# Kernel optimization log

Hardware: AMD Instinct MI355X
Metric: run time of the kernel (lower is better)

The kernel has to match this reference:

```python
import jax, jax.numpy as jnp
import numpy as np

B, Q, C, N, H, W = 2, 4096, 256, 6, 64, 96
HEADS, POINTS = 8, 4


def _grid_sample(img, grid):
    # img: [G, C, H, W]; grid: [G, P, 2] in [-1,1]
    # bilinear, align_corners=False, padding_mode='zeros' (matches F.grid_sample)
    G, Cc, Hh, Ww = img.shape
    gx = (grid[..., 0] + 1.0) * (Ww / 2.0) - 0.5
    gy = (grid[..., 1] + 1.0) * (Hh / 2.0) - 0.5
    x0f = jnp.floor(gx)
    y0f = jnp.floor(gy)
    wx = (gx - x0f)[:, None, :]
    wy = (gy - y0f)[:, None, :]
    x0 = x0f.astype(jnp.int32)
    y0 = y0f.astype(jnp.int32)
    flat = img.reshape(G, Cc, Hh * Ww)

    def gather(xi, yi):
        valid = ((xi >= 0) & (xi < Ww) & (yi >= 0) & (yi < Hh))
        idx = jnp.clip(yi, 0, Hh - 1) * Ww + jnp.clip(xi, 0, Ww - 1)
        v = jnp.take_along_axis(flat, idx[:, None, :], axis=2)  # [G,C,P]
        return v * valid[:, None, :].astype(img.dtype)

    v00 = gather(x0, y0)
    v01 = gather(x0 + 1, y0)
    v10 = gather(x0, y0 + 1)
    v11 = gather(x0 + 1, y0 + 1)
    return (v00 * (1 - wx) * (1 - wy) + v01 * wx * (1 - wy)
            + v10 * (1 - wx) * wy + v11 * wx * wy)


def setup_inputs() -> dict:
    key = jax.random.key(0)
    ks = jax.random.split(key, 12)
    query = jax.random.normal(ks[0], (B, Q, C), dtype=jnp.float32)
    query_coords = jax.random.uniform(ks[1], (B, Q, 3), dtype=jnp.float32)
    image_feats = jax.random.normal(ks[2], (B, N, C, H, W), dtype=jnp.float32)
    # realistic f-theta fisheye intrinsics for 1280x1080 images
    Kmat = np.array([[500.0, 0.0, 640.0], [0.0, 500.0, 540.0], [0.0, 0.0, 1.0]], dtype=np.float32)
    intrinsics = jnp.asarray(np.tile(Kmat, (B, N, 1, 1)))
    # inverse extrinsics: identity rotation, cameras 3m behind the voxel volume (cam_z > 0)
    E = np.tile(np.eye(4, dtype=np.float32), (B, N, 1, 1))
    for n in range(N):
        E[:, n, 0, 3] = 0.2 * n - 0.5
        E[:, n, 2, 3] = 3.0
    inv_extrinsics = jnp.asarray(E)
    s = 1.0 / np.sqrt(C)
    W_off = jax.random.normal(ks[3], (C, N * HEADS * POINTS * 2), dtype=jnp.float32) * 0.02
    b_off = jnp.zeros((N * HEADS * POINTS * 2,), dtype=jnp.float32)
    W_attn = jax.random.normal(ks[4], (C, N * HEADS * POINTS), dtype=jnp.float32) * s
    b_attn = jnp.zeros((N * HEADS * POINTS,), dtype=jnp.float32)
    W_val = jax.random.normal(ks[5], (C, C), dtype=jnp.float32) * s
    b_val = jax.random.normal(ks[6], (C,), dtype=jnp.float32) * 0.01
    W_out = jax.random.normal(ks[7], (C, C), dtype=jnp.float32) * s
    b_out = jax.random.normal(ks[8], (C,), dtype=jnp.float32) * 0.01
    return {"query": query, "query_coords": query_coords, "image_feats": image_feats,
            "intrinsics": intrinsics, "inv_extrinsics": inv_extrinsics,
            "W_off": W_off, "b_off": b_off, "W_attn": W_attn, "b_attn": b_attn,
            "W_val": W_val, "b_val": b_val, "W_out": W_out, "b_out": b_out}


def reference(query, query_coords, image_feats, intrinsics, inv_extrinsics,
              W_off, b_off, W_attn, b_attn, W_val, b_val, W_out, b_out):
    Bq, Qq, Cq = query.shape
    _, Nn, _, Hh, Ww = image_feats.shape
    hd = Cq // HEADS
    # ---- reference points: voxel coords -> world -> camera -> f-theta image ----
    xmin, ymin, zmin, xmax, ymax, zmax = -3.6, -3.0, -0.7, 3.6, 3.0, 2.5
    rx = query_coords[..., 0] * (xmax - xmin) + xmin
    ry = query_coords[..., 1] * (ymax - ymin) + ymin
    rz = query_coords[..., 2] * (zmax - zmin) + zmin
    world = jnp.stack([rx, ry, rz, jnp.ones_like(rx)], axis=-1)  # [B,Q,4]
    cam = jnp.einsum('bnij,bqj->bnqi', inv_extrinsics, world)    # [B,N,Q,4]
    cxp, cyp, czp = cam[..., 0], cam[..., 1], cam[..., 2]
    r3d = jnp.sqrt(cxp * cxp + cyp * cyp + 1e-8)
    theta = jnp.arctan2(r3d, czp)
    phi = jnp.arctan2(cyp, cxp)
    fx = intrinsics[:, :, 0, 0][..., None]
    cx0 = intrinsics[:, :, 0, 2][..., None]
    cy0 = intrinsics[:, :, 1, 2][..., None]
    r_img = fx * theta
    u = r_img * jnp.cos(phi) + cx0
    v = r_img * jnp.sin(phi) + cy0
    origH, origW = 1080, 1280
    ref = jnp.stack([2.0 * u / (origW - 1) - 1.0, 2.0 * v / (origH - 1) - 1.0], axis=-1)  # [B,N,Q,2]
    fov = ((czp > 0) & (theta < 1.372)).astype(query.dtype)      # [B,N,Q]
    # ---- offsets + attention weights ----
    offs = jnp.tanh((query @ W_off + b_off).reshape(Bq, Qq, Nn, HEADS, POINTS, 2)) * 0.5
    aw = (query @ W_attn + b_attn).reshape(Bq, Qq, Nn, HEADS, POINTS)
    aw = aw * jnp.transpose(fov, (0, 2, 1))[..., None, None]
    aw = jax.nn.softmax(aw, axis=-1)
    # ---- value projection ----
    val = jnp.einsum('bnchw,cd->bnhwd', image_feats, W_val) + b_val  # [B,N,H,W,C]
    val = val.reshape(Bq, Nn, Hh, Ww, HEADS, hd)
    # ---- sampling locations ----
    locs = ref[:, :, :, None, None, :] + jnp.transpose(offs, (0, 2, 1, 3, 4, 5))  # [B,N,Q,h,p,2]
    v_all = jnp.transpose(val, (0, 1, 4, 5, 2, 3)).reshape(Bq * Nn * HEADS, hd, Hh, Ww)
    locs_all = jnp.transpose(locs, (0, 1, 3, 2, 4, 5)).reshape(Bq * Nn * HEADS, Qq * POINTS, 2)
    sampled = _grid_sample(v_all, locs_all).reshape(Bq, Nn, HEADS, hd, Qq, POINTS)
    sampled = jnp.transpose(sampled, (0, 4, 1, 2, 5, 3))  # [B,Q,N,heads,points,hd]
    weighted = jnp.sum(sampled * aw[..., None], axis=4)   # [B,Q,N,heads,hd]
    out = weighted.sum(axis=2).reshape(Bq, Qq, Cq)
    return out @ W_out + b_out
```

## Files before the change

kernel.cpp:

```cpp
#include <hip/hip_runtime.h>
#include <math.h>

#define Bb 2
#define Qq 4096
#define Cc 256
#define Nn 6
#define Hh 64
#define Ww 96
#define HEADS 8
#define POINTS 4
#define HW (Hh*Ww)
#define BQ (Bb*Qq)

#define WS_VAL   0
#define WS_WTF   9437184
#define WS_WCHF  9469952
#define WS_WCLF  9543680
#define WS_WOTF  9617408
#define WS_LOCS  18874368
#define WS_AW    22020096
#define WS_REFF  23592960
#define WS_WSUM  23740416

typedef __attribute__((ext_vector_type(8))) short short8;
typedef __attribute__((ext_vector_type(4))) float f32x4;

__device__ __forceinline__ unsigned short f2bf(float f) {
    union { float f; unsigned u; } v; v.f = f;
    unsigned r = (v.u + 0x7fffu + ((v.u >> 16) & 1u)) >> 16;
    return (unsigned short)r;
}
__device__ __forceinline__ float bf2f(unsigned short h) { return __uint_as_float((unsigned)h << 16); }
__device__ __forceinline__ float bflo(unsigned u) { return __uint_as_float(u << 16); }
__device__ __forceinline__ float bfhi(unsigned u) { return __uint_as_float(u & 0xffff0000u); }
__device__ __forceinline__ unsigned packbf(float a, float b) {
    return (unsigned)f2bf(a) | ((unsigned)f2bf(b) << 16);
}

__global__ void prep_kernel(const float* __restrict__ qc,
                            const float* __restrict__ intr,
                            const float* __restrict__ invE,
                            float* __restrict__ reff,
                            const float* __restrict__ Wv,
                            const float* __restrict__ Wo,
                            const float* __restrict__ Wa,
                            const float* __restrict__ Wu,
                            unsigned short* __restrict__ Wtf,
                            unsigned short* __restrict__ Wchf,
                            unsigned short* __restrict__ Wclf,
                            unsigned short* __restrict__ Wotf) {
    int blk = blockIdx.x;
    int tid = threadIdx.x;
    if (blk < 32) {
        int idx = blk * 256 + tid;
        int b = idx >> 12;
        int q = idx & (Qq - 1);
        float rx = qc[idx*3+0] * 7.2f - 3.6f;
        float ry = qc[idx*3+1] * 6.0f - 3.0f;
        float rz = qc[idx*3+2] * 3.2f - 0.7f;
        for (int n = 0; n < Nn; ++n) {
            const float* E = invE + (b*Nn+n)*16;
            float camx = E[0]*rx + E[1]*ry + E[2]*rz  + E[3];
            float camy = E[4]*rx + E[5]*ry + E[6]*rz  + E[7];
            float camz = E[8]*rx + E[9]*ry + E[10]*rz + E[11];
            const float* K = intr + (b*Nn+n)*9;
            float fx = K[0], cx0 = K[2], cy0 = K[5];
            float r3d   = sqrtf(camx*camx + camy*camy + 1e-8f);
            float theta = atan2f(r3d, camz);
            float phi   = atan2f(camy, camx);
            float r_img = fx * theta;
            float u = r_img * cosf(phi) + cx0;
            float v = r_img * sinf(phi) + cy0;
            int base = ((b*Nn+n)*Qq + q)*3;
            reff[base+0] = 2.0f * u / 1279.0f - 1.0f;
            reff[base+1] = 2.0f * v / 1079.0f - 1.0f;
            reff[base+2] = (camz > 0.0f && theta < 1.372f) ? 1.0f : 0.0f;
        }
        return;
    }
    int idx = (blk - 32) * 256 + tid;
    if (idx < 65536) {
        int s = idx & 7, l = (idx >> 3) & 63, kk = (idx >> 9) & 7, t = idx >> 12;
        int n = t*16 + (l & 15);
        int k = kk*32 + (l >> 4)*8 + s;
        Wtf[idx] = f2bf(Wv[k*256 + n]);
    } else if (idx < 212992) {
        int i2 = idx - 65536;
        int s = i2 & 7, l = (i2 >> 3) & 63, kk = (i2 >> 9) & 7, t = i2 >> 12;
        int n = t*16 + (l & 15);
        int k = kk*32 + (l >> 4)*8 + s;
        float w = (n < 384) ? Wo[k*384 + n] : Wa[k*192 + (n - 384)];
        unsigned short h = f2bf(w);
        Wchf[i2] = h;
        Wclf[i2] = f2bf(w - bf2f(h));
    } else {
        int i3 = idx - 212992;
        int s = i3 & 7, l = (i3 >> 3) & 63, kk = (i3 >> 9) & 7, t = i3 >> 12;
        int n = t*16 + (l & 15);
        int k = kk*32 + (l >> 4)*8 + s;
        Wotf[i3] = f2bf(Wu[k*256 + n]);
    }
}

__global__ __launch_bounds__(512, 2) void vp_mfma_kernel(const float* __restrict__ feats,
                                                         const unsigned short* __restrict__ Wtf,
                                                         const float* __restrict__ bv,
                                                         unsigned short* __restrict__ val) {
    __shared__ __align__(16) unsigned short As[64 * 272];
    int t = threadIdx.x;
    int pix0 = blockIdx.x * 64;
    int bn = blockIdx.y;
    const float* A = feats + (size_t)bn * Cc * HW + pix0;
    int lane = t & 63, wavei = t >> 6, quad = lane >> 4, l15 = lane & 15;
    {
        int pq = t & 15;
        int oct = t >> 4;
        float va[8][4];
#pragma unroll
        for (int j = 0; j < 8; ++j)
            *(float4*)va[j] = *(const float4*)&A[(size_t)(oct*8 + j)*HW + pq*4];
#pragma unroll
        for (int e = 0; e < 4; ++e) {
            int m = pq*4 + e;
            uint4 pk;
            pk.x = packbf(va[0][e], va[1][e]);
            pk.y = packbf(va[2][e], va[3][e]);
            pk.z = packbf(va[4][e], va[5][e]);
            pk.w = packbf(va[6][e], va[7][e]);
            *(uint4*)&As[m*264 + oct*8] = pk;
        }
    }
    __syncthreads();
    int wm = wavei & 1;
    int wn = wavei >> 1;
    int r0 = wm*32 + l15, r1 = r0 + 16;
    const unsigned short* Wl = Wtf + (size_t)lane * 8;
#define VP_BOFF(nt, kk) ((size_t)(((wn*4 + (nt))*8 + (kk)) << 9))
    f32x4 acc[2][4];
#pragma unroll
    for (int i = 0; i < 2; ++i)
#pragma unroll
        for (int j = 0; j < 4; ++j) acc[i][j] = (f32x4){0.f, 0.f, 0.f, 0.f};
    short8 bA[4], bB[4];
#pragma unroll
    for (int nt = 0; nt < 4; ++nt) bA[nt] = *(const short8*)&Wl[VP_BOFF(nt, 0)];
#pragma unroll
    for (int kk = 0; kk < 8; kk += 2) {
        if (kk + 1 < 8) {
#pragma unroll
            for (int nt = 0; nt < 4; ++nt) bB[nt] = *(const short8*)&Wl[VP_BOFF(nt, kk+1)];
        }
        {
            short8 a0 = *(const short8*)&As[r0*264 + kk*32 + quad*8];
            short8 a1 = *(const short8*)&As[r1*264 + kk*32 + quad*8];
#pragma unroll
            for (int nt = 0; nt < 4; ++nt) {
                acc[0][nt] = __builtin_amdgcn_mfma_f32_16x16x32_bf16(a0, bA[nt], acc[0][nt], 0, 0, 0);
                acc[1][nt] = __builtin_amdgcn_mfma_f32_16x16x32_bf16(a1, bA[nt], acc[1][nt], 0, 0, 0);
            }
        }
        if (kk + 2 < 8) {
#pragma unroll
            for (int nt = 0; nt < 4; ++nt) bA[nt] = *(const short8*)&Wl[VP_BOFF(nt, kk+2)];
        }
        if (kk + 1 < 8) {
            int k1 = kk + 1;
            short8 a0 = *(const short8*)&As[r0*264 + k1*32 + quad*8];
            short8 a1 = *(const short8*)&As[r1*264 + k1*32 + quad*8];
#pragma unroll
            for (int nt = 0; nt < 4; ++nt) {
                acc[0][nt] = __builtin_amdgcn_mfma_f32_16x16x32_bf16(a0, bB[nt], acc[0][nt], 0, 0, 0);
                acc[1][nt] = __builtin_amdgcn_mfma_f32_16x16x32_bf16(a1, bB[nt], acc[1][nt], 0, 0, 0);
            }
        }
    }
    __syncthreads();
#pragma unroll
    for (int nt = 0; nt < 4; ++nt) {
        int n = wn*64 + nt*16 + l15;
        float bias = bv[n];
#pragma unroll
        for (int mt = 0; mt < 2; ++mt) {
#pragma unroll
            for (int r = 0; r < 4; ++r) {
                int mm = wm*32 + mt*16 + quad*4 + r;
                As[mm*272 + n] = f2bf(acc[mt][nt][r] + bias);
            }
        }
    }
    __syncthreads();
#pragma unroll
    for (int i = 0; i < 4; ++i) {
        int flat = wavei*2048 + i*512 + lane*8;
        int pix = flat >> 8, ch = flat & 255;
        int head = ch >> 5, c32 = ch & 31;
        *(uint4*)&val[(((size_t)bn*HEADS + head)*HW + pix0 + pix)*32 + c32] =
            *(const uint4*)&As[pix*272 + ch];
    }
}

__global__ __launch_bounds__(512, 4) void qp_kernel(const float* __restrict__ query,
                                                    const unsigned short* __restrict__ Wchf,
                                                    const unsigned short* __restrict__ Wclf,
                                                    const float* __restrict__ b_off,
                                                    const float* __restrict__ b_attn,
                                                    const float* __restrict__ reff,
                                                    float* __restrict__ locs,
                                                    float* __restrict__ aw) {
    __shared__ __align__(16) unsigned short Ah[32 * 256];
    __shared__ __align__(16) unsigned short Al[32 * 256];
    int t = threadIdx.x;
    int row0 = blockIdx.x * 32;
    int ty = blockIdx.y;
    {
        int row = t & 31;
        int c2 = t >> 5;
        const float* src = query + (size_t)(row0 + row) * 256;
#pragma unroll
        for (int cc = 0; cc < 2; ++cc) {
            int c = c2 * 2 + cc;
            float4 v0 = *(const float4*)&src[c*8 + 0];
            float4 v1 = *(const float4*)&src[c*8 + 4];
            float f[8] = {v0.x, v0.y, v0.z, v0.w, v1.x, v1.y, v1.z, v1.w};
            unsigned short h[8], l[8];
#pragma unroll
            for (int j = 0; j < 8; ++j) {
                h[j] = f2bf(f[j]);
                l[j] = f2bf(f[j] - bf2f(h[j]));
            }
            uint4 ph, pl;
            ph.x = h[0] | ((unsigned)h[1] << 16); ph.y = h[2] | ((unsigned)h[3] << 16);
            ph.z = h[4] | ((unsigned)h[5] << 16); ph.w = h[6] | ((unsigned)h[7] << 16);
            pl.x = l[0] | ((unsigned)l[1] << 16); pl.y = l[2] | ((unsigned)l[3] << 16);
            pl.z = l[4] | ((unsigned)l[5] << 16); pl.w = l[6] | ((unsigned)l[7] << 16);
            int pos = row * 256 + ((c ^ row) << 3);
            *(uint4*)&Ah[pos] = ph;
            *(uint4*)&Al[pos] = pl;
        }
    }
    __syncthreads();
    int wave = t >> 6, lane = t & 63, quad = lane >> 4, l15 = lane & 15;
    int ms = wave & 1;
    int ng = wave >> 1;
    int arow = ms*16 + l15;
    int bq = row0 >> 12;
    int tile0 = ty*12 + ng*3;
    f32x4 acc[3];
#pragma unroll
    for (int i = 0; i < 3; ++i) acc[i] = (f32x4){0.f, 0.f, 0.f, 0.f};

#define QP_FB(i, kk) (((size_t)((tile0 + (i))*8 + (kk)) << 9) + lane*8)

    if (ty < 2) {
        short8 bhA[3], blA[3], bhB[3], blB[3];
#pragma unroll
        for (int i = 0; i < 3; ++i) {
            bhA[i] = *(const short8*)&Wchf[QP_FB(i, 0)];
            blA[i] = *(const short8*)&Wclf[QP_FB(i, 0)];
        }
#pragma unroll
        for (int kk = 0; kk < 8; kk += 2) {
            if (kk + 1 < 8) {
#pragma unroll
                for (int i = 0; i < 3; ++i) {
                    bhB[i] = *(const short8*)&Wchf[QP_FB(i, kk+1)];
                    blB[i] = *(const short8*)&Wclf[QP_FB(i, kk+1)];
                }
            }
            {
                int apos = arow*256 + (((kk*4+quad) ^ arow) << 3);
                short8 a_h = *(const short8*)&Ah[apos];
                short8 a_l = *(const short8*)&Al[apos];
#pragma unroll
                for (int i = 0; i < 3; ++i) {
                    acc[i] = __builtin_amdgcn_mfma_f32_16x16x32_bf16(a_h, bhA[i], acc[i], 0, 0, 0);
                    acc[i] = __builtin_amdgcn_mfma_f32_16x16x32_bf16(a_l, bhA[i], acc[i], 0, 0, 0);
                    acc[i] = __builtin_amdgcn_mfma_f32_16x16x32_bf16(a_h, blA[i], acc[i], 0, 0, 0);
                }
            }
            if (kk + 2 < 8) {
#pragma unroll
                for (int i = 0; i < 3; ++i) {
                    bhA[i] = *(const short8*)&Wchf[QP_FB(i, kk+2)];
                    blA[i] = *(const short8*)&Wclf[QP_FB(i, kk+2)];
                }
            }
            if (kk + 1 < 8) {
                int k1 = kk + 1;
                int apos = arow*256 + (((k1*4+quad) ^ arow) << 3);
                short8 a_h = *(const short8*)&Ah[apos];
                short8 a_l = *(const short8*)&Al[apos];
#pragma unroll
                for (int i = 0; i < 3; ++i) {
                    acc[i] = __builtin_amdgcn_mfma_f32_16x16x32_bf16(a_h, bhB[i], acc[i], 0, 0, 0);
                    acc[i] = __builtin_amdgcn_mfma_f32_16x16x32_bf16(a_l, bhB[i], acc[i], 0, 0, 0);
                    acc[i] = __builtin_amdgcn_mfma_f32_16x16x32_bf16(a_h, blB[i], acc[i], 0, 0, 0);
                }
            }
        }
#pragma unroll
        for (int i = 0; i < 3; ++i) {
            int j = (tile0 + i)*16 + l15;
            int n_cam = j >> 6;
            int xy = j & 1;
            float bias = b_off[j];
#pragma unroll
            for (int r = 0; r < 4; ++r) {
                int q = row0 + ms*16 + quad*4 + r;
                int qq = q & (Qq-1);
                float refv = reff[((bq*Nn + n_cam)*Qq + qq)*3 + xy];
                locs[(size_t)q*384 + j] = refv + tanhf(acc[i][r] + bias) * 0.5f;
            }
        }
    } else {
        short8 bhA[3], bhB[3];
#pragma unroll
        for (int i = 0; i < 3; ++i) bhA[i] = *(const short8*)&Wchf[QP_FB(i, 0)];
#pragma unroll
        for (int kk = 0; kk < 8; kk += 2) {
            if (kk + 1 < 8) {
#pragma unroll
                for (int i = 0; i < 3; ++i) bhB[i] = *(const short8*)&Wchf[QP_FB(i, kk+1)];
            }
            {
                int apos = arow*256 + (((kk*4+quad) ^ arow) << 3);
                short8 a_h = *(const short8*)&Ah[apos];
#pragma unroll
                for (int i = 0; i < 3; ++i)
                    acc[i] = __builtin_amdgcn_mfma_f32_16x16x32_bf16(a_h, bhA[i], acc[i], 0, 0, 0);
            }
            if (kk + 2 < 8) {
#pragma unroll
                for (int i = 0; i < 3; ++i) bhA[i] = *(const short8*)&Wchf[QP_FB(i, kk+2)];
            }
            if (kk + 1 < 8) {
                int k1 = kk + 1;
                int apos = arow*256 + (((k1*4+quad) ^ arow) << 3);
                short8 a_h = *(const short8*)&Ah[apos];
#pragma unroll
                for (int i = 0; i < 3; ++i)
                    acc[i] = __builtin_amdgcn_mfma_f32_16x16x32_bf16(a_h, bhB[i], acc[i], 0, 0, 0);
            }
        }
#pragma unroll
        for (int i = 0; i < 3; ++i) {
            int j2 = (tile0 + i)*16 + l15 - 384;
            int n_cam = j2 >> 5;
            float bias = b_attn[j2];
#pragma unroll
            for (int r = 0; r < 4; ++r) {
                int q = row0 + ms*16 + quad*4 + r;
                int qq = q & (Qq-1);
                float fov = reff[((bq*Nn + n_cam)*Qq + qq)*3 + 2];
                float lg = (acc[i][r] + bias) * fov;
                float mx = fmaxf(lg, __shfl_xor(lg, 1));
                mx = fmaxf(mx, __shfl_xor(mx, 2));
                float e = expf(lg - mx);
                float s = e + __shfl_xor(e, 1);
                s = s + __shfl_xor(s, 2);
                aw[(size_t)q*192 + j2] = e / s;
            }
        }
    }
#undef QP_FB
}

__global__ __launch_bounds__(256, 4) void samp_kernel(const unsigned short* __restrict__ val,
                                                      const float* __restrict__ locs,
                                                      const float* __restrict__ aw,
                                                      unsigned short* __restrict__ wsum) {
    __shared__ float swgt[4][4][200];
    __shared__ int   soff[4][4][200];
    int t = threadIdx.x, wv = t >> 6, lane = t & 63;
    int q = blockIdx.x * 4 + wv;
    int b = q >> 12;
#pragma unroll
    for (int j = 0; j < 3; ++j) {
        int s = lane + 64*j;
        float2 xy = *(const float2*)&locs[(size_t)q*384 + 2*s];
        float w = aw[(size_t)q*192 + s];
        float gx = (xy.x + 1.0f)*48.0f - 0.5f;
        float gy = (xy.y + 1.0f)*32.0f - 0.5f;
        float x0f = floorf(gx), y0f = floorf(gy);
        float wx = gx - x0f, wy = gy - y0f;
        int ix = (int)x0f, iy = (int)y0f;
        bool vx0 = (unsigned)ix       < (unsigned)Ww;
        bool vx1 = (unsigned)(ix + 1) < (unsigned)Ww;
        bool vy0 = (unsigned)iy       < (unsigned)Hh;
        bool vy1 = (unsigned)(iy + 1) < (unsigned)Hh;
        int ix0 = min(max(ix, 0), Ww-1), ix1 = min(max(ix+1, 0), Ww-1);
        int iy0 = min(max(iy, 0), Hh-1), iy1 = min(max(iy+1, 0), Hh-1);
        swgt[wv][0][s] = (vx0 && vy0) ? w*(1.0f-wx)*(1.0f-wy) : 0.0f;
        swgt[wv][1][s] = (vx1 && vy0) ? w*wx*(1.0f-wy)        : 0.0f;
        swgt[wv][2][s] = (vx0 && vy1) ? w*(1.0f-wx)*wy        : 0.0f;
        swgt[wv][3][s] = (vx1 && vy1) ? w*wx*wy               : 0.0f;
        soff[wv][0][s] = (iy0*Ww + ix0) * 64;
        soff[wv][1][s] = (iy0*Ww + ix1) * 64;
        soff[wv][2][s] = (iy1*Ww + ix0) * 64;
        soff[wv][3][s] = (iy1*Ww + ix1) * 64;
    }
    __syncthreads();
    int cg   = lane >> 5;
    int head = (lane >> 2) & 7;
    int oc   = lane & 3;
    const char* vbase = (const char*)val + (size_t)(b*Nn*HEADS + head)*HW*64 + oc*16;
    float a[8] = {0.f,0.f,0.f,0.f,0.f,0.f,0.f,0.f};
#pragma unroll
    for (int n = 0; n < Nn; ++n) {
        const char* vb = vbase + (size_t)n*HEADS*HW*64;
#pragma unroll
        for (int p = 0; p < POINTS; ++p) {
            int s = (n*HEADS + head)*POINTS + p;
            float w0 = swgt[wv][cg*2+0][s];
            float w1 = swgt[wv][cg*2+1][s];
            int   o0 = soff[wv][cg*2+0][s];
            int   o1 = soff[wv][cg*2+1][s];
            uint4 u0 = *(const uint4*)(vb + o0);
            uint4 u1 = *(const uint4*)(vb + o1);
            a[0] += w0*bflo(u0.x); a[1] += w0*bfhi(u0.x);
            a[2] += w0*bflo(u0.y); a[3] += w0*bfhi(u0.y);
            a[4] += w0*bflo(u0.z); a[5] += w0*bfhi(u0.z);
            a[6] += w0*bflo(u0.w); a[7] += w0*bfhi(u0.w);
            a[0] += w1*bflo(u1.x); a[1] += w1*bfhi(u1.x);
            a[2] += w1*bflo(u1.y); a[3] += w1*bfhi(u1.y);
            a[4] += w1*bflo(u1.z); a[5] += w1*bfhi(u1.z);
            a[6] += w1*bflo(u1.w); a[7] += w1*bfhi(u1.w);
        }
    }
#pragma unroll
    for (int j = 0; j < 8; ++j) a[j] += __shfl_xor(a[j], 32);
    if (cg == 0) {
        int c = head*32 + oc*8;
        uint4 o;
        o.x = packbf(a[0], a[1]);
        o.y = packbf(a[2], a[3]);
        o.z = packbf(a[4], a[5]);
        o.w = packbf(a[6], a[7]);
        *(uint4*)&wsum[(size_t)q*256 + c] = o;
    }
}

__global__ __launch_bounds__(256) void out_mfma_kernel(const unsigned short* __restrict__ wsum,
                                                       const unsigned short* __restrict__ Wotf,
                                                       const float* __restrict__ b_out,
                                                       float* __restrict__ out) {
    int t = threadIdx.x;
    int row0 = blockIdx.x * 64;
    int col0 = blockIdx.y * 128;
    int wave = t >> 6, lane = t & 63, quad = lane >> 4, l15 = lane & 15;
    int wm = wave & 1;
    int wn = wave >> 1;
    f32x4 acc[2][4];
#pragma unroll
    for (int i = 0; i < 2; ++i)
#pragma unroll
        for (int j = 0; j < 4; ++j) acc[i][j] = (f32x4){0.f, 0.f, 0.f, 0.f};
#pragma unroll
    for (int kk = 0; kk < 8; ++kk) {
        short8 a[2];
#pragma unroll
        for (int mt = 0; mt < 2; ++mt)
            a[mt] = *(const short8*)&wsum[(size_t)(row0 + wm*32 + mt*16 + l15)*256 + kk*32 + quad*8];
#pragma unroll
        for (int nt = 0; nt < 4; ++nt) {
            size_t fb = ((size_t)((blockIdx.y*8 + wn*4 + nt)*8 + kk) << 9) + lane*8;
            short8 bfr = *(const short8*)&Wotf[fb];
            acc[0][nt] = __builtin_amdgcn_mfma_f32_16x16x32_bf16(a[0], bfr, acc[0][nt], 0, 0, 0);
            acc[1][nt] = __builtin_amdgcn_mfma_f32_16x16x32_bf16(a[1], bfr, acc[1][nt], 0, 0, 0);
        }
    }
#pragma unroll
    for (int nt = 0; nt < 4; ++nt) {
        int col = col0 + wn*64 + nt*16 + l15;
        float bias = b_out[col];
#pragma unroll
        for (int mt = 0; mt < 2; ++mt) {
#pragma unroll
            for (int r = 0; r < 4; ++r) {
                int q = row0 + wm*32 + mt*16 + quad*4 + r;
                out[(size_t)q*256 + col] = acc[mt][nt][r] + bias;
            }
        }
    }
}

extern "C" void kernel_launch(void* const* d_in, const int* in_sizes, int n_in,
                              void* d_out, int out_size, void* d_ws, size_t ws_size,
                              hipStream_t stream) {
    const float* query  = (const float*)d_in[0];
    const float* qc     = (const float*)d_in[1];
    const float* feats  = (const float*)d_in[2];
    const float* intr   = (const float*)d_in[3];
    const float* invE   = (const float*)d_in[4];
    const float* W_off  = (const float*)d_in[5];
    const float* b_off  = (const float*)d_in[6];
    const float* W_attn = (const float*)d_in[7];
    const float* b_attn = (const float*)d_in[8];
    const float* W_val  = (const float*)d_in[9];
    const float* b_val  = (const float*)d_in[10];
    const float* W_out  = (const float*)d_in[11];
    const float* b_out  = (const float*)d_in[12];
    float* out = (float*)d_out;
    float* ws  = (float*)d_ws;
    unsigned short* val  = (unsigned short*)(ws + WS_VAL);
    unsigned short* Wtf  = (unsigned short*)(ws + WS_WTF);
    unsigned short* Wchf = (unsigned short*)(ws + WS_WCHF);
    unsigned short* Wclf = (unsigned short*)(ws + WS_WCLF);
    unsigned short* Wotf = (unsigned short*)(ws + WS_WOTF);
    float* locs = ws + WS_LOCS;
    float* aw   = ws + WS_AW;
    float* reff = ws + WS_REFF;
    unsigned short* wsum = (unsigned short*)(ws + WS_WSUM);

    hipLaunchKernelGGL(prep_kernel, dim3(1120), dim3(256), 0, stream,
                       qc, intr, invE, reff, W_val, W_off, W_attn, W_out,
                       Wtf, Wchf, Wclf, Wotf);
    hipLaunchKernelGGL(vp_mfma_kernel, dim3(HW/64, Bb*Nn), dim3(512), 0, stream,
                       feats, Wtf, b_val, val);
    hipLaunchKernelGGL(qp_kernel, dim3(BQ/32, 3), dim3(512), 0, stream,
                       query, Wchf, Wclf, b_off, b_attn, reff, locs, aw);
    hipLaunchKernelGGL(samp_kernel, dim3(BQ/4), dim3(256), 0, stream,
                       val, locs, aw, wsum);
    hipLaunchKernelGGL(out_mfma_kernel, dim3(BQ/64, 2), dim3(256), 0, stream,
                       wsum, Wotf, b_out, out);
}
```

Before: 237.2 us.

## Sort queries by spatial bin so sampling blocks gather nearby pixels

Adds a counting sort of queries into a 3D spatial grid of bins (histogram, scan, scatter kernels). The sampling kernel then processes queries in the permuted order, so neighbouring waves touch nearby projected image locations. The aim is better L2/cache locality for the bilinear gathers from the value tensor. It costs three extra small kernel launches plus a memset, one indirection per wave, and atomics in the histogram and scatter steps.

```diff
diff --git a/kernel.cpp b/kernel.cpp
--- a/kernel.cpp
+++ b/kernel.cpp
@@ -21,6 +21,10 @@
 #define WS_AW    22020096
 #define WS_REFF  23592960
 #define WS_WSUM  23740416
+#define WS_HIST  24788992
+#define WS_BOFF  24791040
+#define WS_BIN   24793088
+#define WS_PERM  24801280
 
 typedef __attribute__((ext_vector_type(8))) short short8;
 typedef __attribute__((ext_vector_type(4))) float f32x4;
@@ -102,6 +106,45 @@
     }
 }
 
+__global__ void bin_kernel(const float* __restrict__ qc,
+                           int* __restrict__ hist, int* __restrict__ bin) {
+    int q = blockIdx.x*256 + threadIdx.x;
+    float x = qc[q*3+0], y = qc[q*3+1], z = qc[q*3+2];
+    int bx = min(15, max(0, (int)(x*16.f)));
+    int by = min(15, max(0, (int)(y*16.f)));
+    int bz = min(7,  max(0, (int)(z*8.f)));
+    int b = q >> 12;
+    int bn = (((b*8 + bz)*16 + by)*16 + bx) & 2047;
+    bin[q] = bn;
+    atomicAdd(&hist[bn], 1);
+}
+
+__global__ void scan_kernel(const int* __restrict__ hist, int* __restrict__ boff) {
+    __shared__ int psum[256];
+    int t = threadIdx.x;
+    int loc[8]; int s = 0;
+#pragma unroll
+    for (int i = 0; i < 8; ++i) { loc[i] = hist[t*8+i]; s += loc[i]; }
+    psum[t] = s;
+    __syncthreads();
+    for (int off = 1; off < 256; off <<= 1) {
+        int v = (t >= off) ? psum[t-off] : 0;
+        __syncthreads();
+        psum[t] += v;
+        __syncthreads();
+    }
+    int base = (t == 0) ? 0 : psum[t-1];
+#pragma unroll
+    for (int i = 0; i < 8; ++i) { boff[t*8+i] = base; base += loc[i]; }
+}
+
+__global__ void scatter_kernel(const int* __restrict__ bin,
+                               int* __restrict__ boff, int* __restrict__ perm) {
+    int q = blockIdx.x*256 + threadIdx.x;
+    int pos = atomicAdd(&boff[bin[q]], 1);
+    perm[pos] = q;
+}
+
 __global__ __launch_bounds__(512, 2) void vp_mfma_kernel(const float* __restrict__ feats,
                                                          const unsigned short* __restrict__ Wtf,
                                                          const float* __restrict__ bv,
@@ -368,11 +411,12 @@
 __global__ __launch_bounds__(256, 4) void samp_kernel(const unsigned short* __restrict__ val,
                                                       const float* __restrict__ locs,
                                                       const float* __restrict__ aw,
+                                                      const int* __restrict__ perm,
                                                       unsigned short* __restrict__ wsum) {
     __shared__ float swgt[4][4][200];
     __shared__ int   soff[4][4][200];
     int t = threadIdx.x, wv = t >> 6, lane = t & 63;
-    int q = blockIdx.x * 4 + wv;
+    int q = perm[blockIdx.x * 4 + wv];
     int b = q >> 12;
 #pragma unroll
     for (int j = 0; j < 3; ++j) {
@@ -511,7 +555,18 @@
     float* aw   = ws + WS_AW;
     float* reff = ws + WS_REFF;
     unsigned short* wsum = (unsigned short*)(ws + WS_WSUM);
-
+    int* hist = (int*)(ws + WS_HIST);
+    int* boff = (int*)(ws + WS_BOFF);
+    int* bin  = (int*)(ws + WS_BIN);
+    int* perm = (int*)(ws + WS_PERM);
+
+    hipMemsetAsync(hist, 0, 2048*sizeof(int), stream);
+    hipLaunchKernelGGL(bin_kernel, dim3(BQ/256), dim3(256), 0, stream,
+                       qc, hist, bin);
+    hipLaunchKernelGGL(scan_kernel, dim3(1), dim3(256), 0, stream,
+                       hist, boff);
+    hipLaunchKernelGGL(scatter_kernel, dim3(BQ/256), dim3(256), 0, stream,
+                       bin, boff, perm);
     hipLaunchKernelGGL(prep_kernel, dim3(1120), dim3(256), 0, stream,
                        qc, intr, invE, reff, W_val, W_off, W_attn, W_out,
                        Wtf, Wchf, Wclf, Wotf);
@@ -520,7 +575,7 @@
     hipLaunchKernelGGL(qp_kernel, dim3(BQ/32, 3), dim3(512), 0, stream,
                        query, Wchf, Wclf, b_off, b_attn, reff, locs, aw);
     hipLaunchKernelGGL(samp_kernel, dim3(BQ/4), dim3(256), 0, stream,
-                       val, locs, aw, wsum);
+                       val, locs, aw, perm, wsum);
     hipLaunchKernelGGL(out_mfma_kernel, dim3(BQ/64, 2), dim3(256), 0, stream,
                        wsum, Wotf, b_out, out);
 }
```

After: 256.8 us. +8.3%, slower.
